# Kernel optimization log

Measured on AMD Instinct MI355X. Metric: run time of the kernel, lower is better.

The kernel has to match this reference:

```python
import jax, jax.numpy as jnp
import numpy as np

NUM_USERS = 100000
NUM_ITEMS = 50000
N_NODES = NUM_USERS + NUM_ITEMS
D = 64                 # embed_dim (= user/item/cate embed dims)
NNZ = 2400000          # sparse adjacency nnz (avg degree 16)
B = 4096               # batch size
HIST = 50              # item history length (max)
UHIST = 30             # user history length (max)
MC = 5                 # max categories per item
NC = 1000              # num_cates
CONCAT = 3 * D         # 192 = user/item concat dim
INNER = 2 * CONCAT     # 384 = MLP expansion factor 2
NUM_GNN_LAYERS = 3


def setup_inputs() -> dict:
    ks = jax.random.split(jax.random.key(0), 20)
    emb_table = jax.random.normal(ks[0], (N_NODES, D), jnp.float32) * 0.02
    cate_table = jax.random.normal(ks[1], (NC, D), jnp.float32) * 0.02
    adj_rows = jax.random.randint(ks[2], (NNZ,), 0, N_NODES, jnp.int32)
    adj_cols = jax.random.randint(ks[3], (NNZ,), 0, N_NODES, jnp.int32)
    adj_vals = jax.random.uniform(ks[4], (NNZ,), jnp.float32) * (1.0 / 16.0)
    cates = jax.random.randint(ks[5], (NUM_ITEMS, MC), 0, NC, jnp.int32)
    cate_lens = jax.random.randint(ks[6], (NUM_ITEMS,), 1, MC + 1, jnp.int32)
    users = jax.random.randint(ks[7], (B,), 0, NUM_USERS, jnp.int32)
    items = jax.random.randint(ks[8], (B,), 0, NUM_ITEMS, jnp.int32)
    item_history_matrix = jax.random.randint(ks[9], (B, HIST), 0, NUM_ITEMS, jnp.int32)
    item_history_len = jax.random.randint(ks[10], (B,), 1, HIST + 1, jnp.int32)
    user_history_matrix = jax.random.randint(ks[11], (B, UHIST), 0, NUM_USERS, jnp.int32)
    user_history_len = jax.random.randint(ks[12], (B,), 1, UHIST + 1, jnp.int32)
    # 4 PreNormResidual MLP blocks: [user_mlp, user_mlp_2, item_mlp, item_mlp_2]
    mlp_ln_w = jnp.ones((4, CONCAT), jnp.float32)
    mlp_ln_b = jnp.zeros((4, CONCAT), jnp.float32)
    mlp_w1 = jax.random.normal(ks[13], (4, CONCAT, INNER), jnp.float32) * 0.05
    mlp_b1 = jnp.zeros((4, INNER), jnp.float32)
    mlp_w2 = jax.random.normal(ks[14], (4, INNER, CONCAT), jnp.float32) * 0.05
    mlp_b2 = jnp.zeros((4, CONCAT), jnp.float32)
    return dict(emb_table=emb_table, cate_table=cate_table, adj_vals=adj_vals,
                mlp_ln_w=mlp_ln_w, mlp_ln_b=mlp_ln_b, mlp_w1=mlp_w1, mlp_b1=mlp_b1,
                mlp_w2=mlp_w2, mlp_b2=mlp_b2, adj_rows=adj_rows, adj_cols=adj_cols,
                cates=cates, cate_lens=cate_lens, users=users, items=items,
                item_history_matrix=item_history_matrix, item_history_len=item_history_len,
                user_history_matrix=user_history_matrix, user_history_len=user_history_len)


def _avg_pool(emb, lens):
    # emb: [..., L, D], lens: [...] -> masked mean over L (matches average_pooling)
    L = emb.shape[-2]
    mask = (jnp.arange(L) < lens[..., None]).astype(emb.dtype)[..., None]
    s = jnp.sum(emb * mask, axis=-2)
    c = jnp.sum(mask, axis=-2) + 1e-9
    return s / c


def _layernorm(x, w, b, eps=1e-5):
    mu = jnp.mean(x, axis=-1, keepdims=True)
    var = jnp.mean(jnp.square(x - mu), axis=-1, keepdims=True)
    return (x - mu) * jax.lax.rsqrt(var + eps) * w + b


def _forward(emb_table, cate_table, adj_vals, mlp_ln_w, mlp_ln_b, mlp_w1, mlp_b1,
             mlp_w2, mlp_b2, adj_rows, adj_cols, cates, cate_lens, users, items,
             item_history_matrix, item_history_len, user_history_matrix, user_history_len):
    n = emb_table.shape[0]
    # GNN propagation: mean of [e0, e1, e2, e3], e_{k+1} = A @ e_k (SpMM via segment_sum)
    e = emb_table
    acc = emb_table
    for _ in range(NUM_GNN_LAYERS):
        msgs = adj_vals[:, None] * e[adj_cols]          # [nnz, D]
        e = jax.ops.segment_sum(msgs, adj_rows, num_segments=n)
        acc = acc + e
    gnn = acc / float(NUM_GNN_LAYERS + 1)
    # --- user features ---
    static_u = gnn[users]                               # [B, D]
    hist_item = emb_table[item_history_matrix + NUM_USERS]   # [B, H, D]
    hc = cates[item_history_matrix]                     # [B, H, MC]
    hcl = cate_lens[item_history_matrix]                # [B, H]
    hce = cate_table[hc]                                # [B, H, MC, D]
    avg_cate = _avg_pool(hce, hcl)                      # [B, H, D]
    hist_with_cate = jnp.concatenate([hist_item, avg_cate], axis=-1)  # [B, H, 2D]
    user_hist = _avg_pool(hist_with_cate, item_history_len)           # [B, 2D]
    uf = jnp.concatenate([static_u, user_hist], axis=-1)              # [B, 3D]
    # --- item features ---
    static_i = gnn[items + NUM_USERS]                   # [B, D]
    ice = cate_table[cates[items]]                      # [B, MC, D]
    avg_ic = _avg_pool(ice, cate_lens[items])           # [B, D]
    item_with_cate = jnp.concatenate([static_i, avg_ic], axis=-1)     # [B, 2D]
    hu = emb_table[user_history_matrix]                 # [B, Hu, D]
    item_hist = _avg_pool(hu, user_history_len)         # [B, D]
    itf = jnp.concatenate([item_with_cate, item_hist], axis=-1)       # [B, 3D]
    # --- PreNormResidual MLP blocks ---
    def block(x, i):
        y = _layernorm(x, mlp_ln_w[i], mlp_ln_b[i])
        h = jax.nn.relu(y @ mlp_w1[i] + mlp_b1[i])
        return h @ mlp_w2[i] + mlp_b2[i] + x
    ue = block(uf, 0) + block(uf, 1)
    ie = block(itf, 2) + block(itf, 3)
    ue = ue / jnp.maximum(jnp.linalg.norm(ue, axis=-1, keepdims=True), 1e-12)
    ie = ie / jnp.maximum(jnp.linalg.norm(ie, axis=-1, keepdims=True), 1e-12)
    return ue, ie


def reference(emb_table, cate_table, adj_vals, mlp_ln_w, mlp_ln_b, mlp_w1, mlp_b1,
              mlp_w2, mlp_b2, adj_rows, adj_cols, cates, cate_lens, users, items,
              item_history_matrix, item_history_len, user_history_matrix, user_history_len):
    return _forward(emb_table, cate_table, adj_vals, mlp_ln_w, mlp_ln_b, mlp_w1, mlp_b1,
                    mlp_w2, mlp_b2, adj_rows, adj_cols, cates, cate_lens, users, items,
                    item_history_matrix, item_history_len, user_history_matrix, user_history_len)
```

## Files before the change

kernel.cpp:

```cpp
#include <hip/hip_runtime.h>
#include <hip/hip_bf16.h>
#include <cstdint>
#include <cstddef>

#define NU      100000
#define NN      150000
#define DDIM    64
#define NNZ_C   2400000
#define B_C     4096
#define HIST_C  50
#define UHIST_C 30
#define MC_C    5
#define CDIM    192
#define IDIM    384

#define NBUK    1176
#define BCAP    2304
#define SCAP    44
#define VSCALE  262128.0f
#define VINV    (1.0f/262128.0f)
#define EPB     4096
#define EDGEP   586
#define FEAT_BLKS 2048
#define CONV_BLKS2 144
#define EMBC_BLKS 1172
#define SPMM_BLKS 4704
#define MARK_BLKS 704

#define OFF_E1BF   0
#define OFF_E2BF   4816896
#define OFF_EMBBF  9633792
#define OFF_BKT    14433792
#define OFF_BKP    19852800
#define OFF_GCNT   22562304
#define OFF_SFB    22563584
#define OFF_FLAG   22568320
#define OFF_SDEG   22718848
#define OFF_SEDG   22727040
#define OFF_SIDX   23447936
#define OFF_ROWOFF 23598464
#define OFF_RDEG   23748992
#define OFF_UF     23899520
#define OFF_ITF    24685952
#define OFF_W1T    25472384
#define OFF_W2T    25619840
#define OFF_CNT    4816896
#define OFF_OFFA   5506032
#define OFF_YBF    14433792
#define OFF_HBF    16006656
#define OFF_ZU     0
#define OFF_ZI     786432

typedef __bf16 bf16x8 __attribute__((ext_vector_type(8)));
typedef __bf16 bf16x4 __attribute__((ext_vector_type(4)));
typedef float f32x4 __attribute__((ext_vector_type(4)));

__device__ inline float4 ldb(const __bf16* p) {
  bf16x4 v = *(const bf16x4*)p;
  return make_float4((float)v[0], (float)v[1], (float)v[2], (float)v[3]);
}
__device__ inline void stb(__bf16* p, float4 o) {
  bf16x4 v;
  v[0] = (__bf16)o.x; v[1] = (__bf16)o.y; v[2] = (__bf16)o.z; v[3] = (__bf16)o.w;
  *(bf16x4*)p = v;
}

__device__ inline void xr4(float4& a) {
  a.x += __shfl_xor(a.x, 16, 64); a.y += __shfl_xor(a.y, 16, 64);
  a.z += __shfl_xor(a.z, 16, 64); a.w += __shfl_xor(a.w, 16, 64);
  a.x += __shfl_xor(a.x, 32, 64); a.y += __shfl_xor(a.y, 32, 64);
  a.z += __shfl_xor(a.z, 32, 64); a.w += __shfl_xor(a.w, 32, 64);
}

__global__ __launch_bounds__(256) void seedflag_kernel(
    const int* __restrict__ users, const int* __restrict__ items,
    int* __restrict__ sfb, int* __restrict__ sidx, int* __restrict__ flag) {
  int t = blockIdx.x * 256 + threadIdx.x;
  if (t >= 2 * B_C) return;
  int s = (t < B_C) ? users[t] : items[t - B_C] + NU;
  atomicOr(&sfb[s >> 5], (int)(1u << (s & 31)));
  sidx[s] = t;
  flag[s] = 1;
}

__global__ __launch_bounds__(256) void mega_kernel(
    const int* __restrict__ rows, int* __restrict__ cnt,
    const float* __restrict__ emb, const float* __restrict__ cate_table,
    const int* __restrict__ cates, const int* __restrict__ cate_lens,
    const int* __restrict__ items, const int* __restrict__ ihm,
    const int* __restrict__ ihl, const int* __restrict__ uhm,
    const int* __restrict__ uhl, float* __restrict__ uf,
    float* __restrict__ itf,
    const float* __restrict__ w1, const float* __restrict__ w2,
    __bf16* __restrict__ w1t, __bf16* __restrict__ w2t,
    __bf16* __restrict__ embbf) {
  __shared__ float tlds[64 * 65];
  __shared__ int hist[NBUK];
  int blk = blockIdx.x;
  if (blk < EDGEP) {
    int t = threadIdx.x;
    for (int i = t; i < NBUK; i += 256) hist[i] = 0;
    __syncthreads();
    int base = blk * EPB;
#pragma unroll
    for (int k = 0; k < EPB / 256; ++k) {
      int e = base + k * 256 + t;
      if (e < NNZ_C) atomicAdd(&hist[rows[e] >> 7], 1);
    }
    __syncthreads();
    for (int i = t; i < NBUK; i += 256) cnt[(size_t)blk * NBUK + i] = hist[i];
  } else if (blk < EDGEP + FEAT_BLKS) {
    int tid = threadIdx.x;
    int wave = tid >> 6, w = tid & 63, g = w >> 4, li = w & 15;
    int q = (blk - EDGEP) * 4 + wave;
    if (q < B_C) {
      int b = q;
      int len = ihl[b];
      float4 su = {0.f, 0.f, 0.f, 0.f}, sc = {0.f, 0.f, 0.f, 0.f};
      for (int h = g; h < len; h += 4) {
        int it = ihm[b * HIST_C + h];
        const float4 iv = *(const float4*)(emb + ((size_t)NU + it) * DDIM + li * 4);
        su.x += iv.x; su.y += iv.y; su.z += iv.z; su.w += iv.w;
        int cl = cate_lens[it];
        int id[5];
#pragma unroll
        for (int c = 0; c < 5; ++c) id[c] = cates[it * MC_C + c];
        float4 cs = {0.f, 0.f, 0.f, 0.f};
#pragma unroll
        for (int c = 0; c < 5; ++c) {
          if (c < cl) {
            const float4 cv = *(const float4*)(cate_table + (size_t)id[c] * DDIM + li * 4);
            cs.x += cv.x; cs.y += cv.y; cs.z += cv.z; cs.w += cv.w;
          }
        }
        float icl = 1.f / (float)cl;
        sc.x += cs.x * icl; sc.y += cs.y * icl; sc.z += cs.z * icl; sc.w += cs.w * icl;
      }
      xr4(su); xr4(sc);
      float inv = 1.f / (float)len;
      float* urow = uf + (size_t)b * CDIM;
      if (g == 0) {
        float4 o = {su.x * inv, su.y * inv, su.z * inv, su.w * inv};
        *(float4*)(urow + 64 + li * 4) = o;
      } else if (g == 1) {
        float4 o = {sc.x * inv, sc.y * inv, sc.z * inv, sc.w * inv};
        *(float4*)(urow + 128 + li * 4) = o;
      }
    } else {
      int b = q - B_C;
      int it = items[b];
      int cl = cate_lens[it];
      float4 cs = {0.f, 0.f, 0.f, 0.f};
      for (int c = g; c < cl; c += 4) {
        const float4 cv = *(const float4*)(cate_table + (size_t)cates[it * MC_C + c] * DDIM + li * 4);
        cs.x += cv.x; cs.y += cv.y; cs.z += cv.z; cs.w += cv.w;
      }
      int ul = uhl[b];
      float4 hs = {0.f, 0.f, 0.f, 0.f};
      for (int h = g; h < ul; h += 4) {
        const float4 hv = *(const float4*)(emb + (size_t)uhm[b * UHIST_C + h] * DDIM + li * 4);
        hs.x += hv.x; hs.y += hv.y; hs.z += hv.z; hs.w += hv.w;
      }
      xr4(cs); xr4(hs);
      float* irow = itf + (size_t)b * CDIM;
      if (g == 0) {
        float icl = 1.f / (float)cl;
        float4 o = {cs.x * icl, cs.y * icl, cs.z * icl, cs.w * icl};
        *(float4*)(irow + 64 + li * 4) = o;
      } else if (g == 1) {
        float iul = 1.f / (float)ul;
        float4 o = {hs.x * iul, hs.y * iul, hs.z * iul, hs.w * iul};
        *(float4*)(irow + 128 + li * 4) = o;
      }
    }
  } else if (blk < EDGEP + FEAT_BLKS + CONV_BLKS2) {
    int tile = blk - EDGEP - FEAT_BLKS;
    int t = threadIdx.x;
    if (tile < 72) {
      int p = tile / 18, r = tile % 18, kt = r / 6, nt = r % 6;
      int k0 = kt * 64, n0 = nt * 64;
      const float* srcp = w1 + (size_t)p * (CDIM * IDIM);
#pragma unroll
      for (int i = 0; i < 16; ++i) {
        int idx = i * 256 + t;
        int kl = idx >> 6, nl = idx & 63;
        tlds[kl * 65 + nl] = srcp[(size_t)(k0 + kl) * IDIM + n0 + nl];
      }
      __syncthreads();
#pragma unroll
      for (int i = 0; i < 16; ++i) {
        int idx = i * 256 + t;
        int nl = idx >> 6, kl = idx & 63;
        w1t[((size_t)p * IDIM + n0 + nl) * CDIM + k0 + kl] = (__bf16)tlds[kl * 65 + nl];
      }
    } else {
      int t2 = tile - 72;
      int p = t2 / 18, r = t2 % 18, kt = r / 3, nt = r % 3;
      int k0 = kt * 64, n0 = nt * 64;
      const float* srcp = w2 + (size_t)p * (IDIM * CDIM);
#pragma unroll
      for (int i = 0; i < 16; ++i) {
        int idx = i * 256 + t;
        int kl = idx >> 6, nl = idx & 63;
        tlds[kl * 65 + nl] = srcp[(size_t)(k0 + kl) * CDIM + n0 + nl];
      }
      __syncthreads();
#pragma unroll
      for (int i = 0; i < 16; ++i) {
        int idx = i * 256 + t;
        int nl = idx >> 6, kl = idx & 63;
        w2t[((size_t)p * CDIM + n0 + nl) * IDIM + k0 + kl] = (__bf16)tlds[kl * 65 + nl];
      }
    }
  } else {
    int base = (blk - EDGEP - FEAT_BLKS - CONV_BLKS2) * 2048 + threadIdx.x;
#pragma unroll
    for (int k = 0; k < 8; ++k) {
      int gidx = base + k * 256;
      if (gidx < 2400000) {
        float4 v = ((const float4*)emb)[gidx];
        stb(embbf + (size_t)gidx * 4, v);
      }
    }
  }
}

__global__ __launch_bounds__(256) void prefix_kernel(
    const int* __restrict__ cnt, int* __restrict__ offa, int* __restrict__ gcnt) {
  __shared__ int s[EDGEP];
  int bk = blockIdx.x, t = threadIdx.x;
  for (int i = t; i < EDGEP; i += 256) s[i] = cnt[(size_t)i * NBUK + bk];
  __syncthreads();
  for (int off = 1; off < EDGEP; off <<= 1) {
    int i0 = t, i1 = t + 256, i2 = t + 512;
    int v0 = 0, v1 = 0, v2 = 0;
    if (i0 < EDGEP && i0 >= off) v0 = s[i0 - off];
    if (i1 < EDGEP && i1 >= off) v1 = s[i1 - off];
    if (i2 < EDGEP && i2 >= off) v2 = s[i2 - off];
    __syncthreads();
    if (i0 < EDGEP && i0 >= off) s[i0] += v0;
    if (i1 < EDGEP && i1 >= off) s[i1] += v1;
    if (i2 < EDGEP && i2 >= off) s[i2] += v2;
    __syncthreads();
  }
  int basebk = bk * BCAP;
  for (int i = t; i < EDGEP; i += 256) {
    int incl = s[i];
    int c = cnt[(size_t)i * NBUK + bk];
    offa[(size_t)i * NBUK + bk] = basebk + incl - c;
  }
  if (t == 0) gcnt[bk] = s[EDGEP - 1];
}

__global__ __launch_bounds__(512) void scatter_kernel(
    const int* __restrict__ rows, const int* __restrict__ cols,
    const float* __restrict__ vals, const int* __restrict__ offa,
    int2* __restrict__ bkt, const int* __restrict__ sfb,
    const int* __restrict__ sidx, int* __restrict__ sdeg,
    int2* __restrict__ sedg) {
  __shared__ int hist[NBUK];
  __shared__ int lcur[NBUK];
  __shared__ int bas[NBUK];
  __shared__ int2 stg[EPB];
  __shared__ int dstl[EPB];
  int blk = blockIdx.x, t = threadIdx.x;
  int base = blk * EPB;
  int nblk = NNZ_C - base; if (nblk > EPB) nblk = EPB;
  for (int i = t; i < NBUK; i += 512) hist[i] = 0;
  __syncthreads();
  int rr[8], cc[8]; float vf[8];
#pragma unroll
  for (int k = 0; k < 8; ++k) {
    int e = base + k * 512 + t;
    rr[k] = -1;
    if (e < NNZ_C) {
      rr[k] = rows[e]; cc[k] = cols[e]; vf[k] = vals[e];
      atomicAdd(&hist[rr[k] >> 7], 1);
    }
  }
  __syncthreads();
  int i0 = t, i1 = t + 512, i2 = t + 1024;
  int o0 = (i0 < NBUK) ? hist[i0] : 0;
  int o1 = (i1 < NBUK) ? hist[i1] : 0;
  int o2 = (i2 < NBUK) ? hist[i2] : 0;
  for (int off = 1; off < NBUK; off <<= 1) {
    int v0 = 0, v1 = 0, v2 = 0;
    if (i0 < NBUK && i0 >= off) v0 = hist[i0 - off];
    if (i1 < NBUK && i1 >= off) v1 = hist[i1 - off];
    if (i2 < NBUK && i2 >= off) v2 = hist[i2 - off];
    __syncthreads();
    if (i0 < NBUK && i0 >= off) hist[i0] += v0;
    if (i1 < NBUK && i1 >= off) hist[i1] += v1;
    if (i2 < NBUK && i2 >= off) hist[i2] += v2;
    __syncthreads();
  }
  if (i0 < NBUK) { int ex = hist[i0] - o0; lcur[i0] = ex; bas[i0] = offa[(size_t)blk * NBUK + i0] - ex; }
  if (i1 < NBUK) { int ex = hist[i1] - o1; lcur[i1] = ex; bas[i1] = offa[(size_t)blk * NBUK + i1] - ex; }
  if (i2 < NBUK) { int ex = hist[i2] - o2; lcur[i2] = ex; bas[i2] = offa[(size_t)blk * NBUK + i2] - ex; }
  __syncthreads();
#pragma unroll
  for (int k = 0; k < 8; ++k) {
    if (rr[k] >= 0) {
      int bk2 = rr[k] >> 7;
      int sl = atomicAdd(&lcur[bk2], 1);
      int vi = __float_as_int(vf[k]);
      stg[sl] = make_int2(((rr[k] & 127) << 18) | cc[k], vi);
      int dest = bas[bk2] + sl;
      dstl[sl] = ((unsigned)(dest - bk2 * BCAP) < (unsigned)BCAP) ? dest : -1;
      if ((sfb[rr[k] >> 5] >> (rr[k] & 31)) & 1) {
        int si = sidx[rr[k]];
        int p = atomicAdd(&sdeg[si], 1);
        if (p < SCAP) sedg[(size_t)si * SCAP + p] = make_int2(cc[k], vi);
      }
    }
  }
  __syncthreads();
  for (int i = t; i < nblk; i += 512) {
    int d = dstl[i];
    if (d >= 0) bkt[d] = stg[i];
  }
}

__global__ __launch_bounds__(512) void bucket_sort(
    const int2* __restrict__ bkt, unsigned int* __restrict__ bkp,
    const int* __restrict__ gcnt,
    int* __restrict__ rowoff, int* __restrict__ rdeg,
    const int* __restrict__ sdeg, const int2* __restrict__ sedg,
    int* __restrict__ flag) {
  __shared__ int hcnt[128];
  __shared__ int pre[130];
  __shared__ int cur[128];
  int bk = blockIdx.x, t = threadIdx.x;
  if (bk >= NBUK) {
    int t2 = (bk - NBUK) * 512 + t;
    int si = t2 / SCAP, j = t2 - si * SCAP;
    if (si < 2 * B_C) {
      int n = sdeg[si]; if (n > SCAP) n = SCAP;
      if (j < n) flag[sedg[(size_t)si * SCAP + j].x] = 1;
    }
    return;
  }
  int n = gcnt[bk]; if (n > BCAP) n = BCAP;
  size_t base = (size_t)bk * BCAP;
  if (t < 128) hcnt[t] = 0;
  __syncthreads();
  unsigned int epk[5]; int erow[5];
#pragma unroll
  for (int k = 0; k < 5; ++k) {
    int i = k * 512 + t;
    erow[k] = -1;
    if (i < n) {
      int2 e = bkt[base + i];
      int r = (unsigned)e.x >> 18;
      int col = e.x & 0x3FFFF;
      float v = __int_as_float(e.y);
      unsigned int q = (unsigned int)(v * VSCALE + 0.5f);
      if (q > 16383u) q = 16383u;
      epk[k] = ((unsigned int)col << 14) | q;
      erow[k] = r;
      atomicAdd(&hcnt[r], 1);
    }
  }
  __syncthreads();
  if (t == 0) pre[0] = 0;
  if (t < 128) pre[t + 1] = hcnt[t];
  __syncthreads();
  for (int off = 1; off <= 128; off <<= 1) {
    int v = 0;
    if (t <= 128 && t >= off) v = pre[t - off];
    __syncthreads();
    if (t <= 128 && t >= off) pre[t] += v;
    __syncthreads();
  }
  if (t < 128) cur[t] = pre[t];
  __syncthreads();
#pragma unroll
  for (int k = 0; k < 5; ++k) {
    if (erow[k] >= 0) {
      int slot = atomicAdd(&cur[erow[k]], 1);
      bkp[base + slot] = epk[k];
    }
  }
  if (t < 128) {
    rowoff[bk * 128 + t] = (int)base + pre[t];
    rdeg[bk * 128 + t] = hcnt[t];
  }
}

template<int PRED>
__global__ __launch_bounds__(256) void spmm_csr(
    const __bf16* __restrict__ src, __bf16* __restrict__ dst,
    const int* __restrict__ rowoff, const int* __restrict__ rdeg,
    const unsigned int* __restrict__ bkp, const int* __restrict__ flag) {
  int t = threadIdx.x;
  int wave = t >> 6, w = t & 63, g = w >> 4, li = w & 15;
  int la4 = li * 4;
  int row0 = blockIdx.x * 32 + (wave * 4 + g) * 2;
#pragma unroll
  for (int rr = 0; rr < 2; ++rr) {
    int row = row0 + rr;
    if (PRED && flag[row] == 0) continue;
    int off = rowoff[row];
    int n = rdeg[row];
    const unsigned int* ep = bkp + off;
    float4 a0 = {0.f, 0.f, 0.f, 0.f}, a1 = {0.f, 0.f, 0.f, 0.f};
    float4 a2 = {0.f, 0.f, 0.f, 0.f}, a3 = {0.f, 0.f, 0.f, 0.f};
    int j = 0;
    for (; j + 8 <= n; j += 8) {
      unsigned int e0 = ep[j], e1 = ep[j + 1], e2 = ep[j + 2], e3 = ep[j + 3];
      unsigned int e4 = ep[j + 4], e5 = ep[j + 5], e6 = ep[j + 6], e7 = ep[j + 7];
      const float4 s0 = ldb(src + (size_t)(e0 >> 14) * DDIM + la4);
      const float4 s1 = ldb(src + (size_t)(e1 >> 14) * DDIM + la4);
      const float4 s2 = ldb(src + (size_t)(e2 >> 14) * DDIM + la4);
      const float4 s3 = ldb(src + (size_t)(e3 >> 14) * DDIM + la4);
      const float4 s4 = ldb(src + (size_t)(e4 >> 14) * DDIM + la4);
      const float4 s5 = ldb(src + (size_t)(e5 >> 14) * DDIM + la4);
      const float4 s6 = ldb(src + (size_t)(e6 >> 14) * DDIM + la4);
      const float4 s7 = ldb(src + (size_t)(e7 >> 14) * DDIM + la4);
      float v0 = (float)(e0 & 0x3FFFu) * VINV, v1 = (float)(e1 & 0x3FFFu) * VINV;
      float v2 = (float)(e2 & 0x3FFFu) * VINV, v3 = (float)(e3 & 0x3FFFu) * VINV;
      float v4 = (float)(e4 & 0x3FFFu) * VINV, v5 = (float)(e5 & 0x3FFFu) * VINV;
      float v6 = (float)(e6 & 0x3FFFu) * VINV, v7 = (float)(e7 & 0x3FFFu) * VINV;
      a0.x += v0 * s0.x; a0.y += v0 * s0.y; a0.z += v0 * s0.z; a0.w += v0 * s0.w;
      a1.x += v1 * s1.x; a1.y += v1 * s1.y; a1.z += v1 * s1.z; a1.w += v1 * s1.w;
      a2.x += v2 * s2.x; a2.y += v2 * s2.y; a2.z += v2 * s2.z; a2.w += v2 * s2.w;
      a3.x += v3 * s3.x; a3.y += v3 * s3.y; a3.z += v3 * s3.z; a3.w += v3 * s3.w;
      a0.x += v4 * s4.x; a0.y += v4 * s4.y; a0.z += v4 * s4.z; a0.w += v4 * s4.w;
      a1.x += v5 * s5.x; a1.y += v5 * s5.y; a1.z += v5 * s5.z; a1.w += v5 * s5.w;
      a2.x += v6 * s6.x; a2.y += v6 * s6.y; a2.z += v6 * s6.z; a2.w += v6 * s6.w;
      a3.x += v7 * s7.x; a3.y += v7 * s7.y; a3.z += v7 * s7.z; a3.w += v7 * s7.w;
    }
    for (; j + 2 <= n; j += 2) {
      unsigned int e0 = ep[j], e1 = ep[j + 1];
      const float4 s0 = ldb(src + (size_t)(e0 >> 14) * DDIM + la4);
      const float4 s1 = ldb(src + (size_t)(e1 >> 14) * DDIM + la4);
      float v0 = (float)(e0 & 0x3FFFu) * VINV, v1 = (float)(e1 & 0x3FFFu) * VINV;
      a0.x += v0 * s0.x; a0.y += v0 * s0.y; a0.z += v0 * s0.z; a0.w += v0 * s0.w;
      a1.x += v1 * s1.x; a1.y += v1 * s1.y; a1.z += v1 * s1.z; a1.w += v1 * s1.w;
    }
    if (j < n) {
      unsigned int e0 = ep[j];
      const float4 s0 = ldb(src + (size_t)(e0 >> 14) * DDIM + la4);
      float v0 = (float)(e0 & 0x3FFFu) * VINV;
      a0.x += v0 * s0.x; a0.y += v0 * s0.y; a0.z += v0 * s0.z; a0.w += v0 * s0.w;
    }
    float4 o = {a0.x + a1.x + a2.x + a3.x, a0.y + a1.y + a2.y + a3.y,
                a0.z + a1.z + a2.z + a3.z, a0.w + a1.w + a2.w + a3.w};
    stb(dst + (size_t)row * DDIM + la4, o);
  }
}

__global__ __launch_bounds__(256) void seed_finish(
    const float* __restrict__ emb, const __bf16* __restrict__ e1bf,
    const __bf16* __restrict__ e2bf, const int* __restrict__ sidx,
    const int* __restrict__ sdeg, const int2* __restrict__ sedg,
    const int* __restrict__ users, const int* __restrict__ items,
    float* __restrict__ uf, float* __restrict__ itf) {
  int tid = threadIdx.x;
  int wave = tid >> 6, w = tid & 63, g = w >> 4, li = w & 15;
  int qi = blockIdx.x * 16 + wave * 4 + g;
  int s = (qi < B_C) ? users[qi] : items[qi - B_C] + NU;
  int si = sidx[s];
  int n = sdeg[si]; if (n > SCAP) n = SCAP;
  const int2* ep = sedg + (size_t)si * SCAP;
  float4 a0 = {0.f, 0.f, 0.f, 0.f}, a1 = {0.f, 0.f, 0.f, 0.f};
  float4 a2 = {0.f, 0.f, 0.f, 0.f}, a3 = {0.f, 0.f, 0.f, 0.f};
  int j = 0;
  for (; j + 4 <= n; j += 4) {
    int2 e0 = ep[j], e1v = ep[j + 1], e2v = ep[j + 2], e3v = ep[j + 3];
    const float4 s0 = ldb(e2bf + (size_t)e0.x * DDIM + li * 4);
    const float4 s1 = ldb(e2bf + (size_t)e1v.x * DDIM + li * 4);
    const float4 s2 = ldb(e2bf + (size_t)e2v.x * DDIM + li * 4);
    const float4 s3 = ldb(e2bf + (size_t)e3v.x * DDIM + li * 4);
    float v0 = __int_as_float(e0.y), v1 = __int_as_float(e1v.y);
    float v2 = __int_as_float(e2v.y), v3 = __int_as_float(e3v.y);
    a0.x += v0 * s0.x; a0.y += v0 * s0.y; a0.z += v0 * s0.z; a0.w += v0 * s0.w;
    a1.x += v1 * s1.x; a1.y += v1 * s1.y; a1.z += v1 * s1.z; a1.w += v1 * s1.w;
    a2.x += v2 * s2.x; a2.y += v2 * s2.y; a2.z += v2 * s2.z; a2.w += v2 * s2.w;
    a3.x += v3 * s3.x; a3.y += v3 * s3.y; a3.z += v3 * s3.z; a3.w += v3 * s3.w;
  }
  for (; j < n; ++j) {
    int2 e0 = ep[j];
    const float4 s0 = ldb(e2bf + (size_t)e0.x * DDIM + li * 4);
    float v0 = __int_as_float(e0.y);
    a0.x += v0 * s0.x; a0.y += v0 * s0.y; a0.z += v0 * s0.z; a0.w += v0 * s0.w;
  }
  const float4 e0v = *(const float4*)(emb + (size_t)s * DDIM + li * 4);
  const float4 e1r = ldb(e1bf + (size_t)s * DDIM + li * 4);
  const float4 e2r = ldb(e2bf + (size_t)s * DDIM + li * 4);
  float4 o;
  o.x = (e0v.x + e1r.x + e2r.x + a0.x + a1.x + a2.x + a3.x) * 0.25f;
  o.y = (e0v.y + e1r.y + e2r.y + a0.y + a1.y + a2.y + a3.y) * 0.25f;
  o.z = (e0v.z + e1r.z + e2r.z + a0.z + a1.z + a2.z + a3.z) * 0.25f;
  o.w = (e0v.w + e1r.w + e2r.w + a0.w + a1.w + a2.w + a3.w) * 0.25f;
  float* row = (qi < B_C) ? uf + (size_t)qi * CDIM : itf + (size_t)(qi - B_C) * CDIM;
  *(float4*)(row + li * 4) = o;
}

__global__ __launch_bounds__(64) void ln_kernel(
    const float* __restrict__ uf, const float* __restrict__ itf,
    const float* __restrict__ lnw, const float* __restrict__ lnb,
    __bf16* __restrict__ ybf) {
  int b = blockIdx.x, p = blockIdx.y, t = threadIdx.x;
  const float* x = ((p < 2) ? uf : itf) + (size_t)b * CDIM;
  float v0 = x[t], v1 = x[t + 64], v2 = x[t + 128];
  float s = v0 + v1 + v2;
#pragma unroll
  for (int off = 32; off; off >>= 1) s += __shfl_down(s, off, 64);
  float mu = __shfl(s, 0, 64) * (1.f / 192.f);
  float d0 = v0 - mu, d1 = v1 - mu, d2 = v2 - mu;
  float q = d0 * d0 + d1 * d1 + d2 * d2;
#pragma unroll
  for (int off = 32; off; off >>= 1) q += __shfl_down(q, off, 64);
  float var = __shfl(q, 0, 64) * (1.f / 192.f);
  float rs = 1.f / sqrtf(var + 1e-5f);
  __bf16* yo = ybf + ((size_t)p * B_C + b) * CDIM;
  const float* w = lnw + p * CDIM;
  const float* bb = lnb + p * CDIM;
  yo[t]       = (__bf16)(d0 * rs * w[t]       + bb[t]);
  yo[t + 64]  = (__bf16)(d1 * rs * w[t + 64]  + bb[t + 64]);
  yo[t + 128] = (__bf16)(d2 * rs * w[t + 128] + bb[t + 128]);
}

__global__ __launch_bounds__(256) void gemm1_mfma(
    const __bf16* __restrict__ ybf, const __bf16* __restrict__ w1t,
    const float* __restrict__ b1, __bf16* __restrict__ hbf) {
  int p = blockIdx.z;
  const __bf16* A = ybf + (size_t)p * B_C * CDIM;
  const __bf16* Bt = w1t + (size_t)p * IDIM * CDIM;
  int wave = threadIdx.x >> 6, lane = threadIdx.x & 63;
  int q = lane >> 4, n16 = lane & 15;
  int r0 = blockIdx.x * 64 + wave * 16;
  int c0 = blockIdx.y * 64;
  f32x4 acc[4] = {{0.f, 0.f, 0.f, 0.f}, {0.f, 0.f, 0.f, 0.f},
                  {0.f, 0.f, 0.f, 0.f}, {0.f, 0.f, 0.f, 0.f}};
#pragma unroll
  for (int k0 = 0; k0 < CDIM; k0 += 32) {
    bf16x8 a = *(const bf16x8*)(A + (size_t)(r0 + n16) * CDIM + k0 + q * 8);
#pragma unroll
    for (int c = 0; c < 4; ++c) {
      bf16x8 b = *(const bf16x8*)(Bt + (size_t)(c0 + c * 16 + n16) * CDIM + k0 + q * 8);
      acc[c] = __builtin_amdgcn_mfma_f32_16x16x32_bf16(a, b, acc[c], 0, 0, 0);
    }
  }
#pragma unroll
  for (int c = 0; c < 4; ++c) {
    int col = c0 + c * 16 + n16;
    float bias = b1[p * IDIM + col];
#pragma unroll
    for (int r = 0; r < 4; ++r) {
      int row = r0 + q * 4 + r;
      float v = fmaxf(acc[c][r] + bias, 0.f);
      hbf[((size_t)p * B_C + row) * IDIM + col] = (__bf16)v;
    }
  }
}

__global__ __launch_bounds__(256) void gemm2_mfma(
    const __bf16* __restrict__ hbf, const __bf16* __restrict__ w2t,
    const float* __restrict__ b2, const float* __restrict__ uf,
    const float* __restrict__ itf, float* __restrict__ zu, float* __restrict__ zi) {
  int s = blockIdx.z;
  const float* X = s ? itf : uf;
  float* Z = s ? zi : zu;
  int wave = threadIdx.x >> 6, lane = threadIdx.x & 63;
  int q = lane >> 4, n16 = lane & 15;
  int r0 = blockIdx.x * 64 + wave * 16;
  int c0 = blockIdx.y * 64;
  f32x4 acc[4] = {{0.f, 0.f, 0.f, 0.f}, {0.f, 0.f, 0.f, 0.f},
                  {0.f, 0.f, 0.f, 0.f}, {0.f, 0.f, 0.f, 0.f}};
#pragma unroll
  for (int pi = 0; pi < 2; ++pi) {
    int p = s * 2 + pi;
    const __bf16* A = hbf + (size_t)p * B_C * IDIM;
    const __bf16* Bt = w2t + (size_t)p * CDIM * IDIM;
#pragma unroll
    for (int k0 = 0; k0 < IDIM; k0 += 32) {
      bf16x8 a = *(const bf16x8*)(A + (size_t)(r0 + n16) * IDIM + k0 + q * 8);
#pragma unroll
      for (int c = 0; c < 4; ++c) {
        bf16x8 b = *(const bf16x8*)(Bt + (size_t)(c0 + c * 16 + n16) * IDIM + k0 + q * 8);
        acc[c] = __builtin_amdgcn_mfma_f32_16x16x32_bf16(a, b, acc[c], 0, 0, 0);
      }
    }
  }
#pragma unroll
  for (int c = 0; c < 4; ++c) {
    int col = c0 + c * 16 + n16;
    float bs = b2[(s * 2) * CDIM + col] + b2[(s * 2 + 1) * CDIM + col];
#pragma unroll
    for (int r = 0; r < 4; ++r) {
      int row = r0 + q * 4 + r;
      float xv = X[(size_t)row * CDIM + col];
      Z[(size_t)row * CDIM + col] = acc[c][r] + bs + 2.f * xv;
    }
  }
}

__global__ __launch_bounds__(64) void norm_kernel(
    const float* __restrict__ zu, const float* __restrict__ zi,
    float* __restrict__ out) {
  int b = blockIdx.x, s = blockIdx.y, t = threadIdx.x;
  const float* z = (s ? zi : zu) + (size_t)b * CDIM;
  float v0 = z[t], v1 = z[t + 64], v2 = z[t + 128];
  float q = v0 * v0 + v1 * v1 + v2 * v2;
#pragma unroll
  for (int off = 32; off; off >>= 1) q += __shfl_down(q, off, 64);
  float n = sqrtf(__shfl(q, 0, 64));
  float inv = 1.f / fmaxf(n, 1e-12f);
  float* o = out + (size_t)s * B_C * CDIM + (size_t)b * CDIM;
  o[t] = v0 * inv;
  o[t + 64] = v1 * inv;
  o[t + 128] = v2 * inv;
}

extern "C" void kernel_launch(void* const* d_in, const int* in_sizes, int n_in,
                              void* d_out, int out_size, void* d_ws, size_t ws_size,
                              hipStream_t stream) {
  const float* emb   = (const float*)d_in[0];
  const float* cate  = (const float*)d_in[1];
  const float* avals = (const float*)d_in[2];
  const float* lnw   = (const float*)d_in[3];
  const float* lnb   = (const float*)d_in[4];
  const float* w1    = (const float*)d_in[5];
  const float* b1    = (const float*)d_in[6];
  const float* w2    = (const float*)d_in[7];
  const float* b2    = (const float*)d_in[8];
  const int* arows   = (const int*)d_in[9];
  const int* acols   = (const int*)d_in[10];
  const int* cates_  = (const int*)d_in[11];
  const int* clens   = (const int*)d_in[12];
  const int* users   = (const int*)d_in[13];
  const int* items   = (const int*)d_in[14];
  const int* ihm     = (const int*)d_in[15];
  const int* ihl     = (const int*)d_in[16];
  const int* uhm     = (const int*)d_in[17];
  const int* uhl     = (const int*)d_in[18];
  float* out = (float*)d_out;

  float* W = (float*)d_ws;
  __bf16* e1bf  = (__bf16*)(W + OFF_E1BF);
  __bf16* e2bf  = (__bf16*)(W + OFF_E2BF);
  __bf16* embbf = (__bf16*)(W + OFF_EMBBF);
  int2*   bkt   = (int2*)(W + OFF_BKT);
  unsigned int* bkp = (unsigned int*)(W + OFF_BKP);
  int*    gcnt  = (int*)(W + OFF_GCNT);
  int*    sfb   = (int*)(W + OFF_SFB);
  int*    flag  = (int*)(W + OFF_FLAG);
  int*    sdeg  = (int*)(W + OFF_SDEG);
  int2*   sedg  = (int2*)(W + OFF_SEDG);
  int*    sidx  = (int*)(W + OFF_SIDX);
  int*    rowoff= (int*)(W + OFF_ROWOFF);
  int*    rdeg  = (int*)(W + OFF_RDEG);
  float*  uf    = W + OFF_UF;
  float*  itf   = W + OFF_ITF;
  __bf16* w1t   = (__bf16*)(W + OFF_W1T);
  __bf16* w2t   = (__bf16*)(W + OFF_W2T);
  int*    cnt   = (int*)(W + OFF_CNT);
  int*    offa  = (int*)(W + OFF_OFFA);
  __bf16* ybf   = (__bf16*)(W + OFF_YBF);
  __bf16* hbf   = (__bf16*)(W + OFF_HBF);
  float*  zu    = W + OFF_ZU;
  float*  zi    = W + OFF_ZI;

  (void)hipMemsetAsync(sfb, 0, (size_t)(OFF_SEDG - OFF_SFB) * sizeof(int), stream);

  seedflag_kernel<<<(2 * B_C + 255) / 256, 256, 0, stream>>>(users, items, sfb, sidx, flag);

  mega_kernel<<<EDGEP + FEAT_BLKS + CONV_BLKS2 + EMBC_BLKS, 256, 0, stream>>>(
      arows, cnt,
      emb, cate, cates_, clens, items, ihm, ihl, uhm, uhl, uf, itf,
      w1, w2, w1t, w2t, embbf);

  prefix_kernel<<<NBUK, 256, 0, stream>>>(cnt, offa, gcnt);

  scatter_kernel<<<EDGEP, 512, 0, stream>>>(arows, acols, avals, offa, bkt,
                                            sfb, sidx, sdeg, sedg);

  bucket_sort<<<NBUK + MARK_BLKS, 512, 0, stream>>>(bkt, bkp, gcnt, rowoff, rdeg,
                                                    sdeg, sedg, flag);

  spmm_csr<0><<<SPMM_BLKS, 256, 0, stream>>>(embbf, e1bf, rowoff, rdeg, bkp, flag);
  spmm_csr<1><<<SPMM_BLKS, 256, 0, stream>>>(e1bf, e2bf, rowoff, rdeg, bkp, flag);

  seed_finish<<<(2 * B_C) / 16, 256, 0, stream>>>(emb, e1bf, e2bf, sidx, sdeg,
                                                  sedg, users, items, uf, itf);

  ln_kernel<<<dim3(B_C, 4), 64, 0, stream>>>(uf, itf, lnw, lnb, ybf);
  gemm1_mfma<<<dim3(B_C / 64, IDIM / 64, 4), 256, 0, stream>>>(ybf, w1t, b1, hbf);
  gemm2_mfma<<<dim3(B_C / 64, CDIM / 64, 2), 256, 0, stream>>>(hbf, w2t, b2, uf, itf, zu, zi);
  norm_kernel<<<dim3(B_C, 2), 64, 0, stream>>>(zu, zi, out);
}
```

Measured before the change: 399.2 us.

## Fuse histogram with seed-flag kernel, prefix into mega kernel, shrink bucket records

The edge histogram now runs in the same launch as seed flagging, and the per-bucket prefix scan moves into the mega kernel next to feature pooling, weight conversion and the bf16 embedding cast. This removes one launch and lets independent work overlap. The scatter stage now quantizes values and packs column and value into a 4-byte word plus a 1-byte local row, replacing the 8-byte int2 records. That cuts scatter write and sort read traffic, at the cost of an extra byte-array store.

```diff
diff --git a/kernel.cpp b/kernel.cpp
--- a/kernel.cpp
+++ b/kernel.cpp
@@ -21,6 +21,8 @@
 #define VINV    (1.0f/262128.0f)
 #define EPB     4096
 #define EDGEP   586
+#define SEED_BLKS 32
+#define PFX_BLKS  1176
 #define FEAT_BLKS 2048
 #define CONV_BLKS2 144
 #define EMBC_BLKS 1172
@@ -30,20 +32,21 @@
 #define OFF_E1BF   0
 #define OFF_E2BF   4816896
 #define OFF_EMBBF  9633792
-#define OFF_BKT    14433792
-#define OFF_BKP    19852800
-#define OFF_GCNT   22562304
-#define OFF_SFB    22563584
-#define OFF_FLAG   22568320
-#define OFF_SDEG   22718848
-#define OFF_SEDG   22727040
-#define OFF_SIDX   23447936
-#define OFF_ROWOFF 23598464
-#define OFF_RDEG   23748992
-#define OFF_UF     23899520
-#define OFF_ITF    24685952
-#define OFF_W1T    25472384
-#define OFF_W2T    25619840
+#define OFF_BKP4   14433792
+#define OFF_BROW   17143296
+#define OFF_BKP    17820672
+#define OFF_GCNT   20530176
+#define OFF_SFB    20531456
+#define OFF_FLAG   20536192
+#define OFF_SDEG   20686720
+#define OFF_SEDG   20694912
+#define OFF_SIDX   21415808
+#define OFF_ROWOFF 21566336
+#define OFF_RDEG   21716864
+#define OFF_UF     21867392
+#define OFF_ITF    22653824
+#define OFF_W1T    23440256
+#define OFF_W2T    23587712
 #define OFF_CNT    4816896
 #define OFF_OFFA   5506032
 #define OFF_YBF    14433792
@@ -72,19 +75,36 @@
   a.z += __shfl_xor(a.z, 32, 64); a.w += __shfl_xor(a.w, 32, 64);
 }
 
-__global__ __launch_bounds__(256) void seedflag_kernel(
+__global__ __launch_bounds__(256) void histseed_kernel(
+    const int* __restrict__ rows, int* __restrict__ cnt,
     const int* __restrict__ users, const int* __restrict__ items,
     int* __restrict__ sfb, int* __restrict__ sidx, int* __restrict__ flag) {
-  int t = blockIdx.x * 256 + threadIdx.x;
-  if (t >= 2 * B_C) return;
-  int s = (t < B_C) ? users[t] : items[t - B_C] + NU;
-  atomicOr(&sfb[s >> 5], (int)(1u << (s & 31)));
-  sidx[s] = t;
-  flag[s] = 1;
+  __shared__ int hist[NBUK];
+  int blk = blockIdx.x;
+  if (blk < EDGEP) {
+    int t = threadIdx.x;
+    for (int i = t; i < NBUK; i += 256) hist[i] = 0;
+    __syncthreads();
+    int base = blk * EPB;
+#pragma unroll
+    for (int k = 0; k < EPB / 256; ++k) {
+      int e = base + k * 256 + t;
+      if (e < NNZ_C) atomicAdd(&hist[rows[e] >> 7], 1);
+    }
+    __syncthreads();
+    for (int i = t; i < NBUK; i += 256) cnt[(size_t)blk * NBUK + i] = hist[i];
+  } else {
+    int t2 = (blk - EDGEP) * 256 + threadIdx.x;
+    if (t2 >= 2 * B_C) return;
+    int s = (t2 < B_C) ? users[t2] : items[t2 - B_C] + NU;
+    atomicOr(&sfb[s >> 5], (int)(1u << (s & 31)));
+    sidx[s] = t2;
+    flag[s] = 1;
+  }
 }
 
 __global__ __launch_bounds__(256) void mega_kernel(
-    const int* __restrict__ rows, int* __restrict__ cnt,
+    const int* __restrict__ cnt, int* __restrict__ offa, int* __restrict__ gcnt,
     const float* __restrict__ emb, const float* __restrict__ cate_table,
     const int* __restrict__ cates, const int* __restrict__ cate_lens,
     const int* __restrict__ items, const int* __restrict__ ihm,
@@ -95,24 +115,35 @@
     __bf16* __restrict__ w1t, __bf16* __restrict__ w2t,
     __bf16* __restrict__ embbf) {
   __shared__ float tlds[64 * 65];
-  __shared__ int hist[NBUK];
+  __shared__ int s[EDGEP];
   int blk = blockIdx.x;
-  if (blk < EDGEP) {
-    int t = threadIdx.x;
-    for (int i = t; i < NBUK; i += 256) hist[i] = 0;
+  if (blk < PFX_BLKS) {
+    int bk = blk, t = threadIdx.x;
+    for (int i = t; i < EDGEP; i += 256) s[i] = cnt[(size_t)i * NBUK + bk];
     __syncthreads();
-    int base = blk * EPB;
-#pragma unroll
-    for (int k = 0; k < EPB / 256; ++k) {
-      int e = base + k * 256 + t;
-      if (e < NNZ_C) atomicAdd(&hist[rows[e] >> 7], 1);
-    }
-    __syncthreads();
-    for (int i = t; i < NBUK; i += 256) cnt[(size_t)blk * NBUK + i] = hist[i];
-  } else if (blk < EDGEP + FEAT_BLKS) {
+    for (int off = 1; off < EDGEP; off <<= 1) {
+      int i0 = t, i1 = t + 256, i2 = t + 512;
+      int v0 = 0, v1 = 0, v2 = 0;
+      if (i0 < EDGEP && i0 >= off) v0 = s[i0 - off];
+      if (i1 < EDGEP && i1 >= off) v1 = s[i1 - off];
+      if (i2 < EDGEP && i2 >= off) v2 = s[i2 - off];
+      __syncthreads();
+      if (i0 < EDGEP && i0 >= off) s[i0] += v0;
+      if (i1 < EDGEP && i1 >= off) s[i1] += v1;
+      if (i2 < EDGEP && i2 >= off) s[i2] += v2;
+      __syncthreads();
+    }
+    int basebk = bk * BCAP;
+    for (int i = t; i < EDGEP; i += 256) {
+      int incl = s[i];
+      int c = cnt[(size_t)i * NBUK + bk];
+      offa[(size_t)i * NBUK + bk] = basebk + incl - c;
+    }
+    if (t == 0) gcnt[bk] = s[EDGEP - 1];
+  } else if (blk < PFX_BLKS + FEAT_BLKS) {
     int tid = threadIdx.x;
     int wave = tid >> 6, w = tid & 63, g = w >> 4, li = w & 15;
-    int q = (blk - EDGEP) * 4 + wave;
+    int q = (blk - PFX_BLKS) * 4 + wave;
     if (q < B_C) {
       int b = q;
       int len = ihl[b];
@@ -173,8 +204,8 @@
         *(float4*)(irow + 128 + li * 4) = o;
       }
     }
-  } else if (blk < EDGEP + FEAT_BLKS + CONV_BLKS2) {
-    int tile = blk - EDGEP - FEAT_BLKS;
+  } else if (blk < PFX_BLKS + FEAT_BLKS + CONV_BLKS2) {
+    int tile = blk - PFX_BLKS - FEAT_BLKS;
     int t = threadIdx.x;
     if (tile < 72) {
       int p = tile / 18, r = tile % 18, kt = r / 6, nt = r % 6;
@@ -213,7 +244,7 @@
       }
     }
   } else {
-    int base = (blk - EDGEP - FEAT_BLKS - CONV_BLKS2) * 2048 + threadIdx.x;
+    int base = (blk - PFX_BLKS - FEAT_BLKS - CONV_BLKS2) * 2048 + threadIdx.x;
 #pragma unroll
     for (int k = 0; k < 8; ++k) {
       int gidx = base + k * 256;
@@ -225,43 +256,18 @@
   }
 }
 
-__global__ __launch_bounds__(256) void prefix_kernel(
-    const int* __restrict__ cnt, int* __restrict__ offa, int* __restrict__ gcnt) {
-  __shared__ int s[EDGEP];
-  int bk = blockIdx.x, t = threadIdx.x;
-  for (int i = t; i < EDGEP; i += 256) s[i] = cnt[(size_t)i * NBUK + bk];
-  __syncthreads();
-  for (int off = 1; off < EDGEP; off <<= 1) {
-    int i0 = t, i1 = t + 256, i2 = t + 512;
-    int v0 = 0, v1 = 0, v2 = 0;
-    if (i0 < EDGEP && i0 >= off) v0 = s[i0 - off];
-    if (i1 < EDGEP && i1 >= off) v1 = s[i1 - off];
-    if (i2 < EDGEP && i2 >= off) v2 = s[i2 - off];
-    __syncthreads();
-    if (i0 < EDGEP && i0 >= off) s[i0] += v0;
-    if (i1 < EDGEP && i1 >= off) s[i1] += v1;
-    if (i2 < EDGEP && i2 >= off) s[i2] += v2;
-    __syncthreads();
-  }
-  int basebk = bk * BCAP;
-  for (int i = t; i < EDGEP; i += 256) {
-    int incl = s[i];
-    int c = cnt[(size_t)i * NBUK + bk];
-    offa[(size_t)i * NBUK + bk] = basebk + incl - c;
-  }
-  if (t == 0) gcnt[bk] = s[EDGEP - 1];
-}
-
 __global__ __launch_bounds__(512) void scatter_kernel(
     const int* __restrict__ rows, const int* __restrict__ cols,
     const float* __restrict__ vals, const int* __restrict__ offa,
-    int2* __restrict__ bkt, const int* __restrict__ sfb,
+    unsigned int* __restrict__ bkp4, unsigned char* __restrict__ brow,
+    const int* __restrict__ sfb,
     const int* __restrict__ sidx, int* __restrict__ sdeg,
     int2* __restrict__ sedg) {
   __shared__ int hist[NBUK];
   __shared__ int lcur[NBUK];
   __shared__ int bas[NBUK];
-  __shared__ int2 stg[EPB];
+  __shared__ unsigned int stg_pk[EPB];
+  __shared__ unsigned char stg_row[EPB];
   __shared__ int dstl[EPB];
   int blk = blockIdx.x, t = threadIdx.x;
   int base = blk * EPB;
@@ -304,7 +310,10 @@
       int bk2 = rr[k] >> 7;
       int sl = atomicAdd(&lcur[bk2], 1);
       int vi = __float_as_int(vf[k]);
-      stg[sl] = make_int2(((rr[k] & 127) << 18) | cc[k], vi);
+      unsigned int q = (unsigned int)(vf[k] * VSCALE + 0.5f);
+      if (q > 16383u) q = 16383u;
+      stg_pk[sl] = ((unsigned int)cc[k] << 14) | q;
+      stg_row[sl] = (unsigned char)(rr[k] & 127);
       int dest = bas[bk2] + sl;
       dstl[sl] = ((unsigned)(dest - bk2 * BCAP) < (unsigned)BCAP) ? dest : -1;
       if ((sfb[rr[k] >> 5] >> (rr[k] & 31)) & 1) {
@@ -317,13 +326,13 @@
   __syncthreads();
   for (int i = t; i < nblk; i += 512) {
     int d = dstl[i];
-    if (d >= 0) bkt[d] = stg[i];
+    if (d >= 0) { bkp4[d] = stg_pk[i]; brow[d] = stg_row[i]; }
   }
 }
 
 __global__ __launch_bounds__(512) void bucket_sort(
-    const int2* __restrict__ bkt, unsigned int* __restrict__ bkp,
-    const int* __restrict__ gcnt,
+    const unsigned int* __restrict__ bkp4, const unsigned char* __restrict__ brow,
+    unsigned int* __restrict__ bkp, const int* __restrict__ gcnt,
     int* __restrict__ rowoff, int* __restrict__ rdeg,
     const int* __restrict__ sdeg, const int2* __restrict__ sedg,
     int* __restrict__ flag) {
@@ -350,15 +359,9 @@
     int i = k * 512 + t;
     erow[k] = -1;
     if (i < n) {
-      int2 e = bkt[base + i];
-      int r = (unsigned)e.x >> 18;
-      int col = e.x & 0x3FFFF;
-      float v = __int_as_float(e.y);
-      unsigned int q = (unsigned int)(v * VSCALE + 0.5f);
-      if (q > 16383u) q = 16383u;
-      epk[k] = ((unsigned int)col << 14) | q;
-      erow[k] = r;
-      atomicAdd(&hcnt[r], 1);
+      epk[k] = bkp4[base + i];
+      erow[k] = brow[base + i];
+      atomicAdd(&hcnt[erow[k]], 1);
     }
   }
   __syncthreads();
@@ -642,8 +645,9 @@
   __bf16* e1bf  = (__bf16*)(W + OFF_E1BF);
   __bf16* e2bf  = (__bf16*)(W + OFF_E2BF);
   __bf16* embbf = (__bf16*)(W + OFF_EMBBF);
-  int2*   bkt   = (int2*)(W + OFF_BKT);
-  unsigned int* bkp = (unsigned int*)(W + OFF_BKP);
+  unsigned int* bkp4 = (unsigned int*)(W + OFF_BKP4);
+  unsigned char* brow = (unsigned char*)(W + OFF_BROW);
+  unsigned int* bkp  = (unsigned int*)(W + OFF_BKP);
   int*    gcnt  = (int*)(W + OFF_GCNT);
   int*    sfb   = (int*)(W + OFF_SFB);
   int*    flag  = (int*)(W + OFF_FLAG);
@@ -665,20 +669,19 @@
 
   (void)hipMemsetAsync(sfb, 0, (size_t)(OFF_SEDG - OFF_SFB) * sizeof(int), stream);
 
-  seedflag_kernel<<<(2 * B_C + 255) / 256, 256, 0, stream>>>(users, items, sfb, sidx, flag);
-
-  mega_kernel<<<EDGEP + FEAT_BLKS + CONV_BLKS2 + EMBC_BLKS, 256, 0, stream>>>(
-      arows, cnt,
+  histseed_kernel<<<EDGEP + SEED_BLKS, 256, 0, stream>>>(arows, cnt, users, items,
+                                                         sfb, sidx, flag);
+
+  mega_kernel<<<PFX_BLKS + FEAT_BLKS + CONV_BLKS2 + EMBC_BLKS, 256, 0, stream>>>(
+      cnt, offa, gcnt,
       emb, cate, cates_, clens, items, ihm, ihl, uhm, uhl, uf, itf,
       w1, w2, w1t, w2t, embbf);
 
-  prefix_kernel<<<NBUK, 256, 0, stream>>>(cnt, offa, gcnt);
-
-  scatter_kernel<<<EDGEP, 512, 0, stream>>>(arows, acols, avals, offa, bkt,
-                                            sfb, sidx, sdeg, sedg);
-
-  bucket_sort<<<NBUK + MARK_BLKS, 512, 0, stream>>>(bkt, bkp, gcnt, rowoff, rdeg,
-                                                    sdeg, sedg, flag);
+  scatter_kernel<<<EDGEP, 512, 0, stream>>>(arows, acols, avals, offa,
+                                            bkp4, brow, sfb, sidx, sdeg, sedg);
+
+  bucket_sort<<<NBUK + MARK_BLKS, 512, 0, stream>>>(bkp4, brow, bkp, gcnt,
+                                                    rowoff, rdeg, sdeg, sedg, flag);
 
   spmm_csr<0><<<SPMM_BLKS, 256, 0, stream>>>(embbf, e1bf, rowoff, rdeg, bkp, flag);
   spmm_csr<1><<<SPMM_BLKS, 256, 0, stream>>>(e1bf, e2bf, rowoff, rdeg, bkp, flag);
```

Result: no change. 392.9 us (-1.6%).
